# Kernel optimization log

Hardware: AMD Instinct MI355X
Metric: run time of the kernel (lower is better)

Reference implementation:

```python
import jax, jax.numpy as jnp
import numpy as np

B, S, NQ, FFN, EMB = 8, 4096, 8, 2048, 512


def setup_inputs() -> dict:
    key = jax.random.key(0)
    k0, k1, k2, k3 = jax.random.split(key, 4)
    x = jax.random.normal(k0, (B, S, NQ), dtype=jnp.float32)
    theta = jax.random.normal(k1, (NQ,), dtype=jnp.float32)  # trainable RY angles
    W1 = jax.random.normal(k2, (NQ, FFN), dtype=jnp.float32) / np.float32(np.sqrt(NQ))
    b1 = jnp.zeros((FFN,), dtype=jnp.float32)
    W2 = jax.random.normal(k3, (FFN, EMB), dtype=jnp.float32) / np.float32(np.sqrt(FFN))
    b2 = jnp.zeros((EMB,), dtype=jnp.float32)
    return {"x": x, "theta": theta, "W1": W1, "b1": b1, "W2": W2, "b2": b2}


def reference(x, theta, W1, b1, W2, b2):
    # Quantum layer: per wire i, state RY(theta_i) RX(x_i) |0>; no entangling gates,
    # so the state is a product state and <PauliZ_i> = cos(x_i) * cos(theta_i) exactly.
    # This fuses the per-token / per-gate simulation loop into one batched expression.
    q = jnp.cos(x) * jnp.cos(theta)                     # [B, S, NQ]
    # Dropout is identity at eval time.
    h = jax.nn.relu(jnp.einsum("bsq,qf->bsf", q, W1) + b1)  # [B, S, FFN]
    out = jnp.einsum("bsf,fe->bse", h, W2) + b2             # [B, S, EMB]
    return out
```

## Files before the change

### kernel.cpp

```cpp
#include <hip/hip_runtime.h>

#define T_TOK 32768
#define NQ    8
#define FFN   2048
#define EMB   512
#define BM    128
#define BN    128
#define BK    32
#define NCHUNK (FFN / BK)
#define HROW  36

typedef __attribute__((ext_vector_type(8))) short  short8;
typedef __attribute__((ext_vector_type(4))) float  float4v;

__device__ __forceinline__ unsigned short f2bf(float f) {
  unsigned int u = __float_as_uint(f);
  u += 0x7fffu + ((u >> 16) & 1u);
  return (unsigned short)(u >> 16);
}

__device__ __forceinline__ unsigned pk2bf(float lo, float hi) {
#if __has_builtin(__builtin_amdgcn_cvt_pk_bf16_f32)
  typedef __attribute__((ext_vector_type(2))) __bf16 bf2;
  bf2 p = __builtin_amdgcn_cvt_pk_bf16_f32(lo, hi);
  return *(unsigned*)&p;
#else
  return (unsigned)f2bf(lo) | ((unsigned)f2bf(hi) << 16);
#endif
}

__device__ __forceinline__ short8 ld_h8(const unsigned short* p) {
  uint2 a = *(const uint2*)p;
  uint2 b = *(const uint2*)(p + 4);
  uint4 u; u.x = a.x; u.y = a.y; u.z = b.x; u.w = b.y;
  return *(short8*)&u;
}

__global__ void prep_all(const float* __restrict__ W1,
                         const float* __restrict__ W2,
                         unsigned short* __restrict__ w1t,
                         unsigned short* __restrict__ w2t) {
  __shared__ float t[32][33];
  const int kb = blockIdx.x * 32;
  const int nb = blockIdx.y * 32;
  const int c = threadIdx.x & 31, r0 = threadIdx.x >> 5;
#pragma unroll
  for (int p = 0; p < 4; ++p) {
    int r = r0 + p * 8;
    t[r][c] = W2[(size_t)(kb + r) * EMB + nb + c];
  }
  __syncthreads();
#pragma unroll
  for (int p = 0; p < 4; ++p) {
    int r = r0 + p * 8;
    w2t[(size_t)(nb + r) * FFN + kb + c] = f2bf(t[c][r]);
  }
  if (blockIdx.x == 0) {
    const int base = blockIdx.y * 1024 + threadIdx.x * 4;
#pragma unroll
    for (int e = 0; e < 4; ++e) {
      int idx = base + e;
      int f = idx >> 3, i = idx & 7;
      w1t[idx] = f2bf(W1[i * FFN + f]);
    }
  }
}

__global__ __launch_bounds__(256, 4) void ffq_main(
    const float* __restrict__ x,
    const float* __restrict__ theta,
    const unsigned short* __restrict__ w1t,
    const float* __restrict__ b1,
    const unsigned short* __restrict__ w2t,
    const float* __restrict__ b2,
    float* __restrict__ out) {

  __shared__ __align__(16) unsigned short w2_lds[2][BN * BK];
  __shared__ __align__(16) unsigned short h_lds[4][32 * HROW];

  const int tid  = threadIdx.x;
  const int wave = tid >> 6;
  const int lane = tid & 63;
  const int l15  = lane & 15;
  const int quad = lane >> 4;
  const int tok0 = blockIdx.x * BM;
  const int n0   = blockIdx.y * BN;

  unsigned short* hb = &h_lds[wave][0];

  float cth[8];
  {
    const float4* tp = (const float4*)theta;
    float4 t0 = tp[0], t1 = tp[1];
    cth[0] = __cosf(t0.x); cth[1] = __cosf(t0.y);
    cth[2] = __cosf(t0.z); cth[3] = __cosf(t0.w);
    cth[4] = __cosf(t1.x); cth[5] = __cosf(t1.y);
    cth[6] = __cosf(t1.z); cth[7] = __cosf(t1.w);
  }
  short8 bq[2];
#pragma unroll
  for (int g = 0; g < 2; ++g) {
    short8 v = (short8){0,0,0,0,0,0,0,0};
    if (lane < 16) {
      int tok = tok0 + 32 * wave + 16 * g + lane;
      const float4* xp = (const float4*)(x + (size_t)tok * NQ);
      float4 x0 = xp[0], x1 = xp[1];
      float q0 = __cosf(x0.x) * cth[0], q1 = __cosf(x0.y) * cth[1];
      float q2 = __cosf(x0.z) * cth[2], q3 = __cosf(x0.w) * cth[3];
      float q4 = __cosf(x1.x) * cth[4], q5 = __cosf(x1.y) * cth[5];
      float q6 = __cosf(x1.z) * cth[6], q7 = __cosf(x1.w) * cth[7];
      uint4 uu;
      uu.x = pk2bf(q0, q1); uu.y = pk2bf(q2, q3);
      uu.z = pk2bf(q4, q5); uu.w = pk2bf(q6, q7);
      v = *(short8*)&uu;
    }
    bq[g] = v;
  }

  const int st_row = tid >> 2;
  const int st_gc  = (tid & 3) ^ ((tid >> 3) & 3);

  auto stage_w2 = [&](int kc_, int b_) {
    const int k0_ = kc_ * BK;
#pragma unroll
    for (int issue = 0; issue < 2; ++issue) {
      const int r = issue * 64 + st_row;
      __builtin_amdgcn_global_load_lds(
          (const __attribute__((address_space(1))) void*)(
              w2t + (size_t)(n0 + r) * FFN + k0_ + st_gc * 8),
          (__attribute__((address_space(3))) void*)(
              &w2_lds[b_][issue * 2048 + tid * 8]),
          16, 0, 0);
    }
  };

  float4v acc[2][8];
#pragma unroll
  for (int i = 0; i < 2; ++i)
#pragma unroll
    for (int j = 0; j < 8; ++j)
      acc[i][j] = (float4v){0.f, 0.f, 0.f, 0.f};

  const int bf_c    = quad ^ ((l15 >> 1) & 3);
  const unsigned short* w2r[2] = {
      &w2_lds[0][l15 * BK + bf_c * 8],
      &w2_lds[1][l15 * BK + bf_c * 8]};
  unsigned short* hw0 = hb + l15 * HROW + quad * 4;
  unsigned short* hw1 = hb + (16 + l15) * HROW + quad * 4;
  const unsigned short* hr0 = hb + l15 * HROW + quad * 8;
  const unsigned short* hr1 = hb + (16 + l15) * HROW + quad * 8;

  stage_w2(0, 0);

#pragma unroll 2
  for (int kc = 0; kc < NCHUNK; ++kc) {
    const int buf = kc & 1;
    const int k0  = kc * BK;
    const int nc  = (kc + 1 < NCHUNK) ? kc + 1 : NCHUNK - 1;
    asm volatile("s_waitcnt vmcnt(0)" ::: "memory");
    __builtin_amdgcn_s_barrier();
    __builtin_amdgcn_sched_barrier(0);

    short8 aw0 = *(const short8*)(w1t + (size_t)(k0 + l15) * NQ);
    short8 aw1 = *(const short8*)(w1t + (size_t)(k0 + 16 + l15) * NQ);
    float4 bi0 = *(const float4*)(b1 + k0 + quad * 4);
    float4 bi1 = *(const float4*)(b1 + k0 + 16 + quad * 4);
    __builtin_amdgcn_sched_barrier(0);

    stage_w2(nc, buf ^ 1);
    __builtin_amdgcn_sched_barrier(0);

    {
      float4v c00 = (float4v){0.f,0.f,0.f,0.f}, c01 = c00, c10 = c00, c11 = c00;
      c00 = __builtin_amdgcn_mfma_f32_16x16x32_bf16(aw0, bq[0], c00, 0, 0, 0);
      c01 = __builtin_amdgcn_mfma_f32_16x16x32_bf16(aw0, bq[1], c01, 0, 0, 0);
      c10 = __builtin_amdgcn_mfma_f32_16x16x32_bf16(aw1, bq[0], c10, 0, 0, 0);
      c11 = __builtin_amdgcn_mfma_f32_16x16x32_bf16(aw1, bq[1], c11, 0, 0, 0);
      float v00[4], v01[4], v10[4], v11[4];
#pragma unroll
      for (int r = 0; r < 4; ++r) {
        float a;
        a = c00[r] + bi0[r]; v00[r] = a > 0.f ? a : 0.f;
        a = c01[r] + bi0[r]; v01[r] = a > 0.f ? a : 0.f;
        a = c10[r] + bi1[r]; v10[r] = a > 0.f ? a : 0.f;
        a = c11[r] + bi1[r]; v11[r] = a > 0.f ? a : 0.f;
      }
      uint2 p;
      p.x = pk2bf(v00[0], v00[1]); p.y = pk2bf(v00[2], v00[3]);
      *(uint2*)(hw0)      = p;
      p.x = pk2bf(v01[0], v01[1]); p.y = pk2bf(v01[2], v01[3]);
      *(uint2*)(hw1)      = p;
      p.x = pk2bf(v10[0], v10[1]); p.y = pk2bf(v10[2], v10[3]);
      *(uint2*)(hw0 + 16) = p;
      p.x = pk2bf(v11[0], v11[1]); p.y = pk2bf(v11[2], v11[3]);
      *(uint2*)(hw1 + 16) = p;
    }

    asm volatile("s_waitcnt lgkmcnt(0)" ::: "memory");
    __builtin_amdgcn_sched_barrier(0);

    __builtin_amdgcn_s_setprio(1);
    {
      short8 af0 = ld_h8(hr0);
      short8 af1 = ld_h8(hr1);
      const unsigned short* wb = w2r[buf];
#pragma unroll
      for (int nt = 0; nt < 8; ++nt) {
        short8 bf = *(const short8*)(wb + nt * 512);
        acc[0][nt] = __builtin_amdgcn_mfma_f32_16x16x32_bf16(
            af0, bf, acc[0][nt], 0, 0, 0);
        acc[1][nt] = __builtin_amdgcn_mfma_f32_16x16x32_bf16(
            af1, bf, acc[1][nt], 0, 0, 0);
      }
    }
    __builtin_amdgcn_s_setprio(0);
  }

  asm volatile("s_waitcnt vmcnt(0)" ::: "memory");

#pragma unroll
  for (int nt = 0; nt < 8; ++nt) {
    const int col = n0 + nt * 16 + l15;
    const float bv = b2[col];
#pragma unroll
    for (int mt = 0; mt < 2; ++mt) {
      const int row0 = tok0 + wave * 32 + mt * 16 + quad * 4;
#pragma unroll
      for (int r = 0; r < 4; ++r) {
        out[(size_t)(row0 + r) * EMB + col] = acc[mt][nt][r] + bv;
      }
    }
  }
}

extern "C" void kernel_launch(void* const* d_in, const int* in_sizes, int n_in,
                              void* d_out, int out_size, void* d_ws, size_t ws_size,
                              hipStream_t stream) {
  const float* x     = (const float*)d_in[0];
  const float* theta = (const float*)d_in[1];
  const float* W1    = (const float*)d_in[2];
  const float* b1    = (const float*)d_in[3];
  const float* W2    = (const float*)d_in[4];
  const float* b2    = (const float*)d_in[5];
  float* out = (float*)d_out;

  unsigned short* w1t = (unsigned short*)d_ws;
  unsigned short* w2t = w1t + FFN * NQ;

  prep_all<<<dim3(FFN / 32, EMB / 32), 256, 0, stream>>>(W1, W2, w1t, w2t);

  dim3 grid(T_TOK / BM, EMB / BN);
  ffq_main<<<grid, 256, 0, stream>>>(x, theta, w1t, b1, w2t, b2, out);
}
```

Measured before the change: 171.6 us.

## Switch to 32x32x16 MFMA, pass hidden tile via permlane32 swap, software-pipeline GEMM1

Both GEMMs now use 32x32x16 bf16 MFMA instead of 16x16x32. The ReLU'd hidden activations are moved into the A-operand layout with permlane32_swap in registers, which drops the per-wave LDS staging buffer and its lgkmcnt wait. GEMM1 for the next chunk is computed after the current chunk's GEMM2, with the bias folded into the accumulator init, so it can overlap with the W2 prefetch. In exchange the larger MFMA tiles use more accumulator registers, and the cross-lane data shuffle must match the MFMA layout exactly.

After: 174.7 us. No clear change (+1.8%).

```diff
diff --git a/kernel.cpp b/kernel.cpp
--- a/kernel.cpp
+++ b/kernel.cpp
@@ -8,10 +8,10 @@
 #define BN    128
 #define BK    32
 #define NCHUNK (FFN / BK)
-#define HROW  36
-
-typedef __attribute__((ext_vector_type(8))) short  short8;
-typedef __attribute__((ext_vector_type(4))) float  float4v;
+
+typedef __attribute__((ext_vector_type(8)))  short short8;
+typedef __attribute__((ext_vector_type(16))) float f32x16;
+typedef __attribute__((ext_vector_type(2)))  unsigned int u32x2;
 
 __device__ __forceinline__ unsigned short f2bf(float f) {
   unsigned int u = __float_as_uint(f);
@@ -29,13 +29,6 @@
 #endif
 }
 
-__device__ __forceinline__ short8 ld_h8(const unsigned short* p) {
-  uint2 a = *(const uint2*)p;
-  uint2 b = *(const uint2*)(p + 4);
-  uint4 u; u.x = a.x; u.y = a.y; u.z = b.x; u.w = b.y;
-  return *(short8*)&u;
-}
-
 __global__ void prep_all(const float* __restrict__ W1,
                          const float* __restrict__ W2,
                          unsigned short* __restrict__ w1t,
@@ -76,17 +69,14 @@
     float* __restrict__ out) {
 
   __shared__ __align__(16) unsigned short w2_lds[2][BN * BK];
-  __shared__ __align__(16) unsigned short h_lds[4][32 * HROW];
 
   const int tid  = threadIdx.x;
   const int wave = tid >> 6;
   const int lane = tid & 63;
-  const int l15  = lane & 15;
-  const int quad = lane >> 4;
+  const int nl   = lane & 31;
+  const int hi   = lane >> 5;
   const int tok0 = blockIdx.x * BM;
   const int n0   = blockIdx.y * BN;
-
-  unsigned short* hb = &h_lds[wave][0];
 
   float cth[8];
   {
@@ -97,34 +87,28 @@
     cth[4] = __cosf(t1.x); cth[5] = __cosf(t1.y);
     cth[6] = __cosf(t1.z); cth[7] = __cosf(t1.w);
   }
-  short8 bq[2];
-#pragma unroll
-  for (int g = 0; g < 2; ++g) {
-    short8 v = (short8){0,0,0,0,0,0,0,0};
-    if (lane < 16) {
-      int tok = tok0 + 32 * wave + 16 * g + lane;
-      const float4* xp = (const float4*)(x + (size_t)tok * NQ);
-      float4 x0 = xp[0], x1 = xp[1];
-      float q0 = __cosf(x0.x) * cth[0], q1 = __cosf(x0.y) * cth[1];
-      float q2 = __cosf(x0.z) * cth[2], q3 = __cosf(x0.w) * cth[3];
-      float q4 = __cosf(x1.x) * cth[4], q5 = __cosf(x1.y) * cth[5];
-      float q6 = __cosf(x1.z) * cth[6], q7 = __cosf(x1.w) * cth[7];
-      uint4 uu;
-      uu.x = pk2bf(q0, q1); uu.y = pk2bf(q2, q3);
-      uu.z = pk2bf(q4, q5); uu.w = pk2bf(q6, q7);
-      v = *(short8*)&uu;
-    }
-    bq[g] = v;
-  }
-
-  const int st_row = tid >> 2;
-  const int st_gc  = (tid & 3) ^ ((tid >> 3) & 3);
-
+  short8 bq;
+  {
+    const float4* xp =
+        (const float4*)(x + (size_t)(tok0 + wave * 32 + nl) * NQ);
+    float4 x0 = xp[0], x1 = xp[1];
+    float q0 = __cosf(x0.x) * cth[0], q1 = __cosf(x0.y) * cth[1];
+    float q2 = __cosf(x0.z) * cth[2], q3 = __cosf(x0.w) * cth[3];
+    float q4 = __cosf(x1.x) * cth[4], q5 = __cosf(x1.y) * cth[5];
+    float q6 = __cosf(x1.z) * cth[6], q7 = __cosf(x1.w) * cth[7];
+    uint4 uu;
+    uu.x = pk2bf(q0, q1); uu.y = pk2bf(q2, q3);
+    uu.z = pk2bf(q4, q5); uu.w = pk2bf(q6, q7);
+    if (hi) { uu.x = 0; uu.y = 0; uu.z = 0; uu.w = 0; }
+    bq = *(short8*)&uu;
+  }
+
+  const int st_gc = (tid & 3) ^ ((tid >> 3) & 3);
   auto stage_w2 = [&](int kc_, int b_) {
     const int k0_ = kc_ * BK;
 #pragma unroll
     for (int issue = 0; issue < 2; ++issue) {
-      const int r = issue * 64 + st_row;
+      const int r = issue * 64 + (tid >> 2);
       __builtin_amdgcn_global_load_lds(
           (const __attribute__((address_space(1))) void*)(
               w2t + (size_t)(n0 + r) * FFN + k0_ + st_gc * 8),
@@ -134,102 +118,107 @@
     }
   };
 
-  float4v acc[2][8];
-#pragma unroll
-  for (int i = 0; i < 2; ++i)
-#pragma unroll
-    for (int j = 0; j < 8; ++j)
-      acc[i][j] = (float4v){0.f, 0.f, 0.f, 0.f};
-
-  const int bf_c    = quad ^ ((l15 >> 1) & 3);
-  const unsigned short* w2r[2] = {
-      &w2_lds[0][l15 * BK + bf_c * 8],
-      &w2_lds[1][l15 * BK + bf_c * 8]};
-  unsigned short* hw0 = hb + l15 * HROW + quad * 4;
-  unsigned short* hw1 = hb + (16 + l15) * HROW + quad * 4;
-  const unsigned short* hr0 = hb + l15 * HROW + quad * 8;
-  const unsigned short* hr1 = hb + (16 + l15) * HROW + quad * 8;
-
-  stage_w2(0, 0);
+  const int swz = (nl >> 1) & 3;
+  const unsigned short* rd0[2];
+  const unsigned short* rd1[2];
+#pragma unroll
+  for (int b = 0; b < 2; ++b) {
+    rd0[b] = &w2_lds[b][nl * 32 + ((0 + hi) ^ swz) * 8];
+    rd1[b] = &w2_lds[b][nl * 32 + ((2 + hi) ^ swz) * 8];
+  }
+
+  f32x16 acc[4];
+#pragma unroll
+  for (int nt = 0; nt < 4; ++nt)
+#pragma unroll
+    for (int r = 0; r < 16; ++r) acc[nt][r] = 0.f;
+
+  short8 afA[2], afB[2];
+  auto gemm1 = [&](short8 aw, const float4* b4, short8& oA, short8& oB) {
+    f32x16 c1;
+#pragma unroll
+    for (int r = 0; r < 16; ++r) c1[r] = b4[r >> 2][r & 3];
+    c1 = __builtin_amdgcn_mfma_f32_32x32x16_bf16(aw, bq, c1, 0, 0, 0);
+    unsigned Q[8];
+#pragma unroll
+    for (int p = 0; p < 8; ++p) {
+      float lo = c1[2 * p]     > 0.f ? c1[2 * p]     : 0.f;
+      float hl = c1[2 * p + 1] > 0.f ? c1[2 * p + 1] : 0.f;
+      Q[p] = pk2bf(lo, hl);
+    }
+    u32x2 s0 = __builtin_amdgcn_permlane32_swap(Q[0], Q[2], false, false);
+    u32x2 s1 = __builtin_amdgcn_permlane32_swap(Q[1], Q[3], false, false);
+    u32x2 s2 = __builtin_amdgcn_permlane32_swap(Q[4], Q[6], false, false);
+    u32x2 s3 = __builtin_amdgcn_permlane32_swap(Q[5], Q[7], false, false);
+    uint4 uA; uA.x = s0[0]; uA.y = s1[0]; uA.z = s0[1]; uA.w = s1[1];
+    uint4 uB; uB.x = s2[0]; uB.y = s3[0]; uB.z = s2[1]; uB.w = s3[1];
+    oA = *(short8*)&uA;
+    oB = *(short8*)&uB;
+  };
+
+  {
+    short8 aw0 = *(const short8*)(w1t + (size_t)nl * NQ);
+    float4 b40[4];
+#pragma unroll
+    for (int g2 = 0; g2 < 4; ++g2)
+      b40[g2] = *(const float4*)(b1 + 8 * g2 + 4 * hi);
+    stage_w2(0, 0);
+    gemm1(aw0, b40, afA[0], afB[0]);
+  }
 
 #pragma unroll 2
   for (int kc = 0; kc < NCHUNK; ++kc) {
-    const int buf = kc & 1;
-    const int k0  = kc * BK;
-    const int nc  = (kc + 1 < NCHUNK) ? kc + 1 : NCHUNK - 1;
+    const int b  = kc & 1;
+    const int nc = (kc + 1 < NCHUNK) ? kc + 1 : NCHUNK - 1;
+
     asm volatile("s_waitcnt vmcnt(0)" ::: "memory");
     __builtin_amdgcn_s_barrier();
     __builtin_amdgcn_sched_barrier(0);
 
-    short8 aw0 = *(const short8*)(w1t + (size_t)(k0 + l15) * NQ);
-    short8 aw1 = *(const short8*)(w1t + (size_t)(k0 + 16 + l15) * NQ);
-    float4 bi0 = *(const float4*)(b1 + k0 + quad * 4);
-    float4 bi1 = *(const float4*)(b1 + k0 + 16 + quad * 4);
-    __builtin_amdgcn_sched_barrier(0);
-
-    stage_w2(nc, buf ^ 1);
-    __builtin_amdgcn_sched_barrier(0);
-
-    {
-      float4v c00 = (float4v){0.f,0.f,0.f,0.f}, c01 = c00, c10 = c00, c11 = c00;
-      c00 = __builtin_amdgcn_mfma_f32_16x16x32_bf16(aw0, bq[0], c00, 0, 0, 0);
-      c01 = __builtin_amdgcn_mfma_f32_16x16x32_bf16(aw0, bq[1], c01, 0, 0, 0);
-      c10 = __builtin_amdgcn_mfma_f32_16x16x32_bf16(aw1, bq[0], c10, 0, 0, 0);
-      c11 = __builtin_amdgcn_mfma_f32_16x16x32_bf16(aw1, bq[1], c11, 0, 0, 0);
-      float v00[4], v01[4], v10[4], v11[4];
-#pragma unroll
-      for (int r = 0; r < 4; ++r) {
-        float a;
-        a = c00[r] + bi0[r]; v00[r] = a > 0.f ? a : 0.f;
-        a = c01[r] + bi0[r]; v01[r] = a > 0.f ? a : 0.f;
-        a = c10[r] + bi1[r]; v10[r] = a > 0.f ? a : 0.f;
-        a = c11[r] + bi1[r]; v11[r] = a > 0.f ? a : 0.f;
-      }
-      uint2 p;
-      p.x = pk2bf(v00[0], v00[1]); p.y = pk2bf(v00[2], v00[3]);
-      *(uint2*)(hw0)      = p;
-      p.x = pk2bf(v01[0], v01[1]); p.y = pk2bf(v01[2], v01[3]);
-      *(uint2*)(hw1)      = p;
-      p.x = pk2bf(v10[0], v10[1]); p.y = pk2bf(v10[2], v10[3]);
-      *(uint2*)(hw0 + 16) = p;
-      p.x = pk2bf(v11[0], v11[1]); p.y = pk2bf(v11[2], v11[3]);
-      *(uint2*)(hw1 + 16) = p;
-    }
-
-    asm volatile("s_waitcnt lgkmcnt(0)" ::: "memory");
-    __builtin_amdgcn_sched_barrier(0);
+    short8 aw = *(const short8*)(w1t + (size_t)(nc * 32 + nl) * NQ);
+    float4 b4[4];
+#pragma unroll
+    for (int g2 = 0; g2 < 4; ++g2)
+      b4[g2] = *(const float4*)(b1 + nc * 32 + 8 * g2 + 4 * hi);
+
+    stage_w2(nc, b ^ 1);
 
     __builtin_amdgcn_s_setprio(1);
     {
-      short8 af0 = ld_h8(hr0);
-      short8 af1 = ld_h8(hr1);
-      const unsigned short* wb = w2r[buf];
-#pragma unroll
-      for (int nt = 0; nt < 8; ++nt) {
-        short8 bf = *(const short8*)(wb + nt * 512);
-        acc[0][nt] = __builtin_amdgcn_mfma_f32_16x16x32_bf16(
-            af0, bf, acc[0][nt], 0, 0, 0);
-        acc[1][nt] = __builtin_amdgcn_mfma_f32_16x16x32_bf16(
-            af1, bf, acc[1][nt], 0, 0, 0);
-      }
+      short8 bf[4];
+#pragma unroll
+      for (int nt = 0; nt < 4; ++nt)
+        bf[nt] = *(const short8*)(rd0[b] + nt * 1024);
+#pragma unroll
+      for (int nt = 0; nt < 4; ++nt)
+        acc[nt] = __builtin_amdgcn_mfma_f32_32x32x16_bf16(
+            afA[b], bf[nt], acc[nt], 0, 0, 0);
+#pragma unroll
+      for (int nt = 0; nt < 4; ++nt)
+        bf[nt] = *(const short8*)(rd1[b] + nt * 1024);
+#pragma unroll
+      for (int nt = 0; nt < 4; ++nt)
+        acc[nt] = __builtin_amdgcn_mfma_f32_32x32x16_bf16(
+            afB[b], bf[nt], acc[nt], 0, 0, 0);
     }
     __builtin_amdgcn_s_setprio(0);
+
+    gemm1(aw, b4, afA[b ^ 1], afB[b ^ 1]);
   }
 
   asm volatile("s_waitcnt vmcnt(0)" ::: "memory");
 
 #pragma unroll
-  for (int nt = 0; nt < 8; ++nt) {
-    const int col = n0 + nt * 16 + l15;
+  for (int nt = 0; nt < 4; ++nt) {
+    const int col = n0 + nt * 32 + nl;
     const float bv = b2[col];
-#pragma unroll
-    for (int mt = 0; mt < 2; ++mt) {
-      const int row0 = tok0 + wave * 32 + mt * 16 + quad * 4;
-#pragma unroll
-      for (int r = 0; r < 4; ++r) {
-        out[(size_t)(row0 + r) * EMB + col] = acc[mt][nt][r] + bv;
-      }
-    }
+    const int rbase = tok0 + wave * 32 + 4 * hi;
+#pragma unroll
+    for (int g2 = 0; g2 < 4; ++g2)
+#pragma unroll
+      for (int rr = 0; rr < 4; ++rr)
+        out[(size_t)(rbase + 8 * g2 + rr) * EMB + col] =
+            acc[nt][4 * g2 + rr] + bv;
   }
 }
 
```
